# Optimization experiments

Measured on AMD Instinct MI355X. Metric: run time of the kernel, lower is better.

The kernel has to match this reference:

```python
import jax, jax.numpy as jnp
import numpy as np

GRID_SIZE = 5
SPLINE_ORDER = 3
N_COEF = GRID_SIZE + SPLINE_ORDER  # 8
NUM_NODES = 100000
NUM_EDGES = 1200000
NUM_GRAPHS = 512
D = 64
N_TARGETS = 10


def _grid():
    # uniform grid on [-1, 1] extended by spline_order knots on each side (efficient-kan default)
    h = 2.0 / GRID_SIZE
    return jnp.arange(-SPLINE_ORDER, GRID_SIZE + SPLINE_ORDER + 1, dtype=jnp.float32) * h - 1.0


def b_splines(x):
    # x: (N, in) -> (N, in, N_COEF) via Cox-de Boor recursion
    g = _grid()
    xe = x[..., None]
    bases = ((xe >= g[:-1]) & (xe < g[1:])).astype(x.dtype)
    for k in range(1, SPLINE_ORDER + 1):
        left = (xe - g[: -(k + 1)]) / (g[k:-1] - g[: -(k + 1)])
        right = (g[k + 1:] - xe) / (g[k + 1:] - g[1:-k])
        bases = left * bases[..., :-1] + right * bases[..., 1:]
    return bases


def kan_linear(x, base_w, spline_w, scaler):
    # efficient-kan KANLinear: silu base branch + standalone-scaled spline branch
    base = jax.nn.silu(x) @ base_w.T
    sb = b_splines(x)  # (N, in, N_COEF)
    spline = jnp.einsum('nig,oig->no', sb, spline_w * scaler[..., None])
    return base + spline


def setup_inputs() -> dict:
    key = jax.random.key(0)
    ks = jax.random.split(key, 12)
    inp = {
        'x': jax.random.normal(ks[0], (NUM_NODES, D), dtype=jnp.float32),
        'edge_index': jax.random.randint(ks[1], (2, NUM_EDGES), 0, NUM_NODES, dtype=jnp.int64),
        'batch': jnp.sort(jax.random.randint(ks[2], (NUM_NODES,), 0, NUM_GRAPHS, dtype=jnp.int64)),
        # GINConv layer 0 KAN (D -> D)
        'base_w0': jax.random.normal(ks[3], (D, D), dtype=jnp.float32) * 0.1,
        'spline_w0': jax.random.normal(ks[4], (D, D, N_COEF), dtype=jnp.float32) * 0.1,
        'scaler0': jax.random.normal(ks[5], (D, D), dtype=jnp.float32) * 0.1 + 1.0,
        # GINConv layer 1 KAN (D -> D)
        'base_w1': jax.random.normal(ks[6], (D, D), dtype=jnp.float32) * 0.1,
        'spline_w1': jax.random.normal(ks[7], (D, D, N_COEF), dtype=jnp.float32) * 0.1,
        'scaler1': jax.random.normal(ks[8], (D, D), dtype=jnp.float32) * 0.1 + 1.0,
        # head KAN (D -> N_TARGETS)
        'base_wh': jax.random.normal(ks[9], (N_TARGETS, D), dtype=jnp.float32) * 0.1,
        'spline_wh': jax.random.normal(ks[10], (N_TARGETS, D, N_COEF), dtype=jnp.float32) * 0.1,
        'scaler_h': jax.random.normal(ks[11], (N_TARGETS, D), dtype=jnp.float32) * 0.1 + 1.0,
    }
    return inp


def reference(x, edge_index, batch, base_w0, spline_w0, scaler0,
              base_w1, spline_w1, scaler1, base_wh, spline_wh, scaler_h):
    src, dst = edge_index[0], edge_index[1]
    n = x.shape[0]
    # GINConv layer 0: nn((1+eps)*x + sum_{j in N(i)} x_j), eps=0; dropout is eval-mode identity
    agg = jax.ops.segment_sum(x[src], dst, num_segments=n)
    h = kan_linear(x + agg, base_w0, spline_w0, scaler0)
    # GINConv layer 1
    agg = jax.ops.segment_sum(h[src], dst, num_segments=n)
    h = kan_linear(h + agg, base_w1, spline_w1, scaler1)
    # global_add_pool over graphs, then KAN head
    pooled = jax.ops.segment_sum(h, batch, num_segments=NUM_GRAPHS)
    return kan_linear(pooled, base_wh, spline_wh, scaler_h)
```

## Files before the change

kernel.cpp:

```cpp
#include <hip/hip_runtime.h>
#include <hip/hip_fp16.h>
#include <math.h>

#define NODES   100000
#define EDGES   1200000
#define GRAPHS  512
#define DIM     64
#define NT      10
#define KTOT    576

#define NB      512
#define NBUSED  391
#define EPB     4096
#define CAP     4608

#define KSTAGE     64
#define WTL_STRIDE 72
#define V_STRIDE   72

#define S3B     ((EDGES + EPB - 1) / EPB)
#define PREPB   ((2 * DIM * KTOT) / 512)
#define CONVB   ((NODES * 16 + 32 + 511) / 512)

typedef _Float16 f16x8  __attribute__((ext_vector_type(8)));
typedef __fp16   fp16x2 __attribute__((ext_vector_type(2)));
typedef __attribute__((ext_vector_type(4))) float frag_cd;

__device__ __forceinline__ float silu(float x) {
    return x * __builtin_amdgcn_rcpf(1.f + __expf(-x));
}

__device__ __forceinline__ unsigned packh2(float a, float b) {
    fp16x2 h = __builtin_amdgcn_cvt_pkrtz(a, b);
    return __builtin_bit_cast(unsigned, h);
}

union H8 { uint4 u; __half2 h[4]; };

__device__ __forceinline__ f16x8 bases_frag(float xv) {
    float tt  = fmaf(xv, 2.5f, 5.5f);
    float fm  = floorf(tt);
    int   m   = (int)fm;
    float u   = tt - fm;
    float u2  = u * u;
    float u3  = u2 * u;
    float v0  = fmaf(fmaf(fmaf(u, -(1.f / 6.f), 0.5f), u, -0.5f), u, 1.f / 6.f);
    float v1  = fmaf(u3, 0.5f, fmaf(u2, -1.f, 2.f / 3.f));
    float v2  = fmaf(u + u2 - u3, 0.5f, 1.f / 6.f);
    float v3  = u3 * (1.f / 6.f);

    unsigned d0 = packh2(v0, v1);
    unsigned d1 = packh2(v2, v3);
    int p = m - 3;
    int B = p >> 1;
    bool odd = (p & 1) != 0;
    unsigned e1 = __builtin_amdgcn_alignbit(d1, d0, 16);
    unsigned W0 = odd ? (d0 << 16) : d0;
    unsigned W1 = odd ? e1 : d1;
    unsigned W2 = odd ? (d1 >> 16) : 0u;
    union { f16x8 f; unsigned u[4]; } r;
    r.u[0] = (B == 0) ? W0 : ((B == -1) ? W1 : ((B == -2) ? W2 : 0u));
    r.u[1] = (B == 1) ? W0 : ((B ==  0) ? W1 : ((B == -1) ? W2 : 0u));
    r.u[2] = (B == 2) ? W0 : ((B ==  1) ? W1 : ((B ==  0) ? W2 : 0u));
    r.u[3] = (B == 3) ? W0 : ((B ==  2) ? W1 : ((B ==  1) ? W2 : 0u));
    return r.f;
}

__global__ __launch_bounds__(512) void mega(const int* __restrict__ ei,
                                            int* __restrict__ bcur,
                                            unsigned* __restrict__ tmp,
                                            const float* __restrict__ bw0,
                                            const float* __restrict__ sw0,
                                            const float* __restrict__ sc0,
                                            const float* __restrict__ bw1,
                                            const float* __restrict__ sw1,
                                            const float* __restrict__ sc1,
                                            unsigned short* __restrict__ wt0,
                                            unsigned short* __restrict__ wt1,
                                            const float* __restrict__ x,
                                            const int* __restrict__ bat,
                                            unsigned short* __restrict__ xb,
                                            unsigned short* __restrict__ hpad,
                                            int* __restrict__ goff) {
    __shared__ int hist[NB], lstart[NB], gbase[NB], cur[NB];
    __shared__ unsigned ebuf[EPB];
    __shared__ unsigned short bk[EPB];
    const int bx = blockIdx.x;
    const int t  = threadIdx.x;

    if (bx < S3B) {
        hist[t] = 0; cur[t] = 0;
        __syncthreads();
        const int e0 = bx * EPB;
        int src[8], dst[8];
#pragma unroll
        for (int k = 0; k < 8; ++k) {
            int e = e0 + t + k * 512;
            bool valid = e < EDGES;
            src[k] = valid ? ei[e] : 0;
            dst[k] = valid ? ei[EDGES + e] : -1;
            if (valid) atomicAdd(&hist[dst[k] >> 8], 1);
        }
        __syncthreads();
        int v = hist[t];
        lstart[t] = v;
        __syncthreads();
        int run = v;
        for (int d = 1; d < NB; d <<= 1) {
            int a = (t >= d) ? lstart[t - d] : 0;
            __syncthreads();
            run += a; lstart[t] = run;
            __syncthreads();
        }
        lstart[t] = run - v;
        if (v) gbase[t] = atomicAdd(&bcur[t], v);
        __syncthreads();
#pragma unroll
        for (int k = 0; k < 8; ++k) {
            if (dst[k] >= 0) {
                int b = dst[k] >> 8;
                int pos = lstart[b] + atomicAdd(&cur[b], 1);
                ebuf[pos] = (unsigned)src[k] | ((unsigned)(dst[k] & 255) << 24);
                bk[pos] = (unsigned short)b;
            }
        }
        __syncthreads();
        int total = EDGES - e0; if (total > EPB) total = EPB;
        for (int i = t; i < total; i += 512) {
            int b = bk[i];
            tmp[(size_t)b * CAP + gbase[b] + (i - lstart[b])] = ebuf[i];
        }
        return;
    }

    if (bx < S3B + PREPB) {
        int idx = (bx - S3B) * 512 + t;
        int layer = idx >= DIM * KTOT;
        int li = layer ? idx - DIM * KTOT : idx;
        const float* bw = layer ? bw1 : bw0;
        const float* sw = layer ? sw1 : sw0;
        const float* sc = layer ? sc1 : sc0;
        unsigned short* wt = layer ? wt1 : wt0;
        int o = li / KTOT, k = li % KTOT;
        float v;
        if (k < DIM) {
            v = bw[o * DIM + k];
        } else {
            int i = (k - DIM) >> 3, g = (k - DIM) & 7;
            v = sw[(o * DIM + i) * 8 + g] * sc[o * DIM + i];
        }
        wt[li] = __half_as_ushort(__float2half(v));
        return;
    }

    int i = (bx - S3B - PREPB) * 512 + t;
    if (i < NODES * 16) {
        float4 v = ((const float4*)x)[i];
        unsigned lo = packh2(v.x, v.y);
        unsigned hi = packh2(v.z, v.w);
        ((uint2*)xb)[i] = make_uint2(lo, hi);
        if ((i & 15) == 0) {
            int n = i >> 4;
            int b  = bat[n];
            int bp = (n == 0) ? -1 : bat[n - 1];
            for (int g = bp + 1; g <= b; ++g) goff[g] = n;
        }
        if (i == 0) {
            int blast = bat[NODES - 1];
            for (int g = blast + 1; g <= GRAPHS; ++g) goff[g] = NODES;
        }
    } else {
        int j = i - NODES * 16;
        if (j < 16)      ((uint2*)xb)[NODES * 16 + j] = make_uint2(0, 0);
        else if (j < 32) ((uint2*)hpad)[j - 16]       = make_uint2(0, 0);
    }
}

__global__ __launch_bounds__(1024) void s4_fill(const unsigned* __restrict__ tmp,
                                                const int* __restrict__ bcur,
                                                int2* __restrict__ rowp,
                                                int* __restrict__ col) {
    __shared__ int deg[256], scanI[256], cur[256];
    __shared__ int tot;
    __shared__ int4 colbuf4[CAP / 4];
    int* colbuf = (int*)colbuf4;
    const int b = blockIdx.x, t = threadIdx.x;
    const int cnt = bcur[b];
    const int base = b * CAP;
    if (t < 256) deg[t] = 0;
    __syncthreads();
    for (int i = t; i < cnt; i += 1024)
        atomicAdd(&deg[tmp[base + i] >> 24], 1);
    __syncthreads();
    if (t < 256) scanI[t] = (deg[t] + 3) & ~3;
    __syncthreads();
    for (int d = 1; d < 256; d <<= 1) {
        int a = 0;
        if (t < 256 && t >= d) a = scanI[t - d];
        __syncthreads();
        if (t < 256) scanI[t] += a;
        __syncthreads();
    }
    if (t < 256) {
        int pad = (deg[t] + 3) & ~3;
        int start = scanI[t] - pad;
        int ng = b * 256 + t;
        if (ng < NODES) rowp[ng] = make_int2(base + start, base + start + pad);
        cur[t] = start;
        if (t == 255) tot = scanI[255];
    }
    __syncthreads();
    for (int i = t; i < cnt; i += 1024) {
        unsigned p = tmp[base + i];
        int pos = atomicAdd(&cur[p >> 24], 1);
        colbuf[pos] = (int)(p & 0xFFFFFFu);
    }
    __syncthreads();
    if (t < 256) {
        int pad = (deg[t] + 3) & ~3;
        int end = scanI[t] - pad + pad;
        for (int k = cur[t]; k < end; ++k) colbuf[k] = NODES;
    }
    __syncthreads();
    int nq = tot >> 2;
    int4* out4 = (int4*)(col + base);
    for (int i = t; i < nq; i += 1024) out4[i] = colbuf4[i];
    if (t < 4) col[base + tot + t] = NODES;
}

__global__ __launch_bounds__(256, 8) void fused_layer(const unsigned short* __restrict__ xin,
                                                      const int2* __restrict__ rowp,
                                                      const int* __restrict__ col,
                                                      const unsigned short* __restrict__ wt,
                                                      unsigned short* __restrict__ out) {
    __shared__ unsigned short wt_lds[64 * WTL_STRIDE];
    __shared__ unsigned short v_lds[64 * V_STRIDE];

    const int t     = threadIdx.x;
    const int nbase = blockIdx.x * 64;

    uint4 p0, p1;
    {
        int c0 = t, c1 = t + 256;
        p0 = *(const uint4*)(wt + (c0 >> 3) * KTOT + (c0 & 7) * 8);
        p1 = *(const uint4*)(wt + (c1 >> 3) * KTOT + (c1 & 7) * 8);
    }

    const uint4* x4 = (const uint4*)xin;
#pragma unroll
    for (int rd = 0; rd < 2; ++rd) {
        int idx  = t + rd * 256;
        int node = idx >> 3, c8 = idx & 7;
        int n = nbase + node;
        uint4 res = make_uint4(0, 0, 0, 0);
        if (n < NODES) {
            int2 be = rowp[n];
            H8 a0, a1, a2, a3;
            a0.u = x4[n * 8 + c8];
            a1.u = make_uint4(0, 0, 0, 0);
            a2.u = make_uint4(0, 0, 0, 0);
            a3.u = make_uint4(0, 0, 0, 0);
            for (int p = be.x; p < be.y; p += 4) {
                int4 c4 = *(const int4*)(col + p);
                H8 r0, r1, r2, r3;
                r0.u = x4[c4.x * 8 + c8];
                r1.u = x4[c4.y * 8 + c8];
                r2.u = x4[c4.z * 8 + c8];
                r3.u = x4[c4.w * 8 + c8];
#pragma unroll
                for (int j = 0; j < 4; ++j) {
                    a0.h[j] = __hadd2(a0.h[j], r0.h[j]);
                    a1.h[j] = __hadd2(a1.h[j], r1.h[j]);
                    a2.h[j] = __hadd2(a2.h[j], r2.h[j]);
                    a3.h[j] = __hadd2(a3.h[j], r3.h[j]);
                }
            }
#pragma unroll
            for (int j = 0; j < 4; ++j)
                a0.h[j] = __hadd2(__hadd2(a0.h[j], a1.h[j]), __hadd2(a2.h[j], a3.h[j]));
            res = a0.u;
        }
        *(uint4*)(v_lds + node * V_STRIDE + c8 * 8) = res;
    }
    {
        int c0 = t, c1 = t + 256;
        *(uint4*)(wt_lds + (c0 >> 3) * WTL_STRIDE + (c0 & 7) * 8) = p0;
        *(uint4*)(wt_lds + (c1 >> 3) * WTL_STRIDE + (c1 & 7) * 8) = p1;
    }
    __syncthreads();

    const int w = t >> 6;
    const int l = t & 63;
    const int q = l >> 4;
    const int c = l & 15;
    const unsigned short* vrow = v_lds + ((w << 4) + c) * V_STRIDE;

    frag_cd ac0 = {0.f, 0.f, 0.f, 0.f};
    frag_cd ac1 = {0.f, 0.f, 0.f, 0.f};
    frag_cd ac2 = {0.f, 0.f, 0.f, 0.f};
    frag_cd ac3 = {0.f, 0.f, 0.f, 0.f};

#define MSTEP(OFF, A) {                                                          \
        f16x8 b0 = *(const f16x8*)(wt_lds + (c     ) * WTL_STRIDE + (OFF));      \
        f16x8 b1 = *(const f16x8*)(wt_lds + (c + 16) * WTL_STRIDE + (OFF));      \
        f16x8 b2 = *(const f16x8*)(wt_lds + (c + 32) * WTL_STRIDE + (OFF));      \
        f16x8 b3 = *(const f16x8*)(wt_lds + (c + 48) * WTL_STRIDE + (OFF));      \
        ac0 = __builtin_amdgcn_mfma_f32_16x16x32_f16(A, b0, ac0, 0, 0, 0);       \
        ac1 = __builtin_amdgcn_mfma_f32_16x16x32_f16(A, b1, ac1, 0, 0, 0);       \
        ac2 = __builtin_amdgcn_mfma_f32_16x16x32_f16(A, b2, ac2, 0, 0, 0);       \
        ac3 = __builtin_amdgcn_mfma_f32_16x16x32_f16(A, b3, ac3, 0, 0, 0); }

    {
        int c0 = t, c1 = t + 256;
        p0 = *(const uint4*)(wt + (c0 >> 3) * KTOT + KSTAGE + (c0 & 7) * 8);
        p1 = *(const uint4*)(wt + (c1 >> 3) * KTOT + KSTAGE + (c1 & 7) * 8);
    }

#pragma unroll
    for (int s = 0; s < 2; ++s) {
        f16x8 hv = *(const f16x8*)(vrow + 32 * s + 8 * q);
        float f[8];
#pragma unroll
        for (int j = 0; j < 8; ++j) f[j] = silu((float)hv[j]);
        union { f16x8 v; unsigned u[4]; } a;
#pragma unroll
        for (int j = 0; j < 4; ++j) a.u[j] = packh2(f[2 * j], f[2 * j + 1]);
        MSTEP(32 * s + 8 * q, a.v);
    }

#pragma unroll
    for (int st = 1; st < 9; ++st) {
        __syncthreads();
        {
            int c0 = t, c1 = t + 256;
            *(uint4*)(wt_lds + (c0 >> 3) * WTL_STRIDE + (c0 & 7) * 8) = p0;
            *(uint4*)(wt_lds + (c1 >> 3) * WTL_STRIDE + (c1 & 7) * 8) = p1;
        }
        __syncthreads();
        if (st < 8) {
            int c0 = t, c1 = t + 256;
            p0 = *(const uint4*)(wt + (c0 >> 3) * KTOT + (st + 1) * KSTAGE + (c0 & 7) * 8);
            p1 = *(const uint4*)(wt + (c1 >> 3) * KTOT + (st + 1) * KSTAGE + (c1 & 7) * 8);
        }
#pragma unroll
        for (int k2 = 0; k2 < 2; ++k2) {
            f16x8 a = bases_frag((float)(*(const _Float16*)(vrow + 8 * (st - 1) + 4 * k2 + q)));
            MSTEP(32 * k2 + 8 * q, a);
        }
    }
#undef MSTEP

    const int n0 = nbase + (w << 4) + (q << 2);
#pragma unroll
    for (int r = 0; r < 4; ++r) {
        int n = n0 + r;
        if (n < NODES) {
            unsigned short* o = out + (size_t)n * DIM + c;
            o[0]  = __half_as_ushort(__float2half(ac0[r]));
            o[16] = __half_as_ushort(__float2half(ac1[r]));
            o[32] = __half_as_ushort(__float2half(ac2[r]));
            o[48] = __half_as_ushort(__float2half(ac3[r]));
        }
    }
}

__global__ __launch_bounds__(256) void pool_head(const unsigned short* __restrict__ h,
                                                 const int* __restrict__ goff,
                                                 const float* __restrict__ bwh,
                                                 const float* __restrict__ swh,
                                                 const float* __restrict__ sch,
                                                 float* __restrict__ out) {
    __shared__ float red[32][64];
    const int g = blockIdx.x, t = threadIdx.x;
    const int start = goff[g], end = goff[g + 1];
    const int grp = t >> 3, c8 = t & 7;
    const uint4* h4 = (const uint4*)h;

    float f[8];
#pragma unroll
    for (int j = 0; j < 8; ++j) f[j] = 0.f;
    for (int n = start + grp; n < end; n += 32) {
        H8 v; v.u = h4[n * 8 + c8];
#pragma unroll
        for (int j = 0; j < 4; ++j) {
            float2 fj = __half22float2(v.h[j]);
            f[2 * j]     += fj.x;
            f[2 * j + 1] += fj.y;
        }
    }
#pragma unroll
    for (int j = 0; j < 8; ++j) red[grp][c8 * 8 + j] = f[j];
    __syncthreads();

    if (t < 64) {
        const int i = t;
        float xv = 0.f;
#pragma unroll
        for (int k = 0; k < 32; ++k) xv += red[k][i];

        float s  = silu(xv);
        float tt  = fmaf(xv, 2.5f, 5.5f);
        float fm  = floorf(tt);
        int   m   = (int)fm;
        float u   = tt - fm;
        float u2  = u * u;
        float u3  = u2 * u;
        float v0  = fmaf(fmaf(fmaf(u, -(1.f / 6.f), 0.5f), u, -0.5f), u, 1.f / 6.f);
        float v1  = fmaf(u3, 0.5f, fmaf(u2, -1.f, 2.f / 3.f));
        float v2  = fmaf(u + u2 - u3, 0.5f, 1.f / 6.f);
        float v3  = u3 * (1.f / 6.f);
        bool inr  = (m >= 0) && (m <= 10);
        float b[8];
#pragma unroll
        for (int j = 0; j < 8; ++j) {
            float bv = 0.f;
            bv = (j == m - 3) ? v0 : bv;
            bv = (j == m - 2) ? v1 : bv;
            bv = (j == m - 1) ? v2 : bv;
            bv = (j == m)     ? v3 : bv;
            b[j] = inr ? bv : 0.f;
        }

        float part[NT];
#pragma unroll
        for (int o = 0; o < NT; ++o) {
            const float* sp = swh + (o * DIM + i) * 8;
            float sb = 0.f;
#pragma unroll
            for (int qq = 0; qq < 8; ++qq) sb = fmaf(b[qq], sp[qq], sb);
            part[o] = fmaf(s, bwh[o * DIM + i], sb * sch[o * DIM + i]);
        }
#pragma unroll
        for (int o = 0; o < NT; ++o) {
            float v = part[o];
#pragma unroll
            for (int off = 32; off > 0; off >>= 1) v += __shfl_down(v, off, 64);
            if (i == 0) out[g * NT + o] = v;
        }
    }
}

extern "C" void kernel_launch(void* const* d_in, const int* in_sizes, int n_in,
                              void* d_out, int out_size, void* d_ws, size_t ws_size,
                              hipStream_t stream) {
    const float* x   = (const float*)d_in[0];
    const int*   ei  = (const int*)d_in[1];
    const int*   bat = (const int*)d_in[2];
    const float* bw0 = (const float*)d_in[3];
    const float* sw0 = (const float*)d_in[4];
    const float* sc0 = (const float*)d_in[5];
    const float* bw1 = (const float*)d_in[6];
    const float* sw1 = (const float*)d_in[7];
    const float* sc1 = (const float*)d_in[8];
    const float* bwh = (const float*)d_in[9];
    const float* swh = (const float*)d_in[10];
    const float* sch = (const float*)d_in[11];
    float* out = (float*)d_out;

    const size_t ROW = (size_t)(NODES + 1) * DIM;

    unsigned short* wt0 = (unsigned short*)d_ws;
    unsigned short* wt1 = wt0 + DIM * KTOT;
    unsigned short* xbf = wt1 + DIM * KTOT;
    unsigned short* hbf = xbf + ROW;
    unsigned short* h2  = hbf + ROW;
    int* goff     = (int*)(h2 + (size_t)NODES * DIM);
    int2* rowp    = (int2*)(goff + 514);
    int* col      = (int*)(rowp + NODES);
    int* bcur     = col + (size_t)NB * CAP;
    unsigned* tmp = (unsigned*)(bcur + NB);

    (void)hipMemsetAsync(bcur, 0, NB * sizeof(int), stream);

    mega<<<S3B + PREPB + CONVB, 512, 0, stream>>>(
        ei, bcur, tmp,
        bw0, sw0, sc0, bw1, sw1, sc1, wt0, wt1,
        x, bat, xbf, hbf + (size_t)NODES * DIM, goff);

    s4_fill<<<NBUSED, 1024, 0, stream>>>(tmp, bcur, rowp, col);

    const int layer_blocks = (NODES + 63) / 64;
    fused_layer<<<layer_blocks, 256, 0, stream>>>(xbf, rowp, col, wt0, hbf);
    fused_layer<<<layer_blocks, 256, 0, stream>>>(hbf, rowp, col, wt1, h2);

    pool_head<<<GRAPHS, 256, 0, stream>>>(h2, goff, bwh, swh, sch, out);
}
```

Before: 198.4 us.

## Replace bucketed LDS edge sort with global-atomic degree count, scan, and scatter CSR

Replaces the two-pass bucketed CSR build with a simpler three-step scheme. Per-node degrees are counted with global atomics inside the mega kernel. A wave-shuffle scan then computes padded row starts per 256-node block, and a separate scatter kernel places source indices using per-node atomic cursors. This removes the LDS histogram/scan/staging and the intermediate tmp buffer, at the cost of an extra kernel launch, many contended global atomics, random global writes, and nondeterministic neighbor order within a row.

```diff
diff --git a/kernel.cpp b/kernel.cpp
--- a/kernel.cpp
+++ b/kernel.cpp
@@ -67,8 +67,7 @@
 }
 
 __global__ __launch_bounds__(512) void mega(const int* __restrict__ ei,
-                                            int* __restrict__ bcur,
-                                            unsigned* __restrict__ tmp,
+                                            int* __restrict__ deg,
                                             const float* __restrict__ bw0,
                                             const float* __restrict__ sw0,
                                             const float* __restrict__ sc0,
@@ -82,53 +81,15 @@
                                             unsigned short* __restrict__ xb,
                                             unsigned short* __restrict__ hpad,
                                             int* __restrict__ goff) {
-    __shared__ int hist[NB], lstart[NB], gbase[NB], cur[NB];
-    __shared__ unsigned ebuf[EPB];
-    __shared__ unsigned short bk[EPB];
     const int bx = blockIdx.x;
     const int t  = threadIdx.x;
 
     if (bx < S3B) {
-        hist[t] = 0; cur[t] = 0;
-        __syncthreads();
-        const int e0 = bx * EPB;
-        int src[8], dst[8];
+        const int e0 = bx * EPB + t;
 #pragma unroll
         for (int k = 0; k < 8; ++k) {
-            int e = e0 + t + k * 512;
-            bool valid = e < EDGES;
-            src[k] = valid ? ei[e] : 0;
-            dst[k] = valid ? ei[EDGES + e] : -1;
-            if (valid) atomicAdd(&hist[dst[k] >> 8], 1);
-        }
-        __syncthreads();
-        int v = hist[t];
-        lstart[t] = v;
-        __syncthreads();
-        int run = v;
-        for (int d = 1; d < NB; d <<= 1) {
-            int a = (t >= d) ? lstart[t - d] : 0;
-            __syncthreads();
-            run += a; lstart[t] = run;
-            __syncthreads();
-        }
-        lstart[t] = run - v;
-        if (v) gbase[t] = atomicAdd(&bcur[t], v);
-        __syncthreads();
-#pragma unroll
-        for (int k = 0; k < 8; ++k) {
-            if (dst[k] >= 0) {
-                int b = dst[k] >> 8;
-                int pos = lstart[b] + atomicAdd(&cur[b], 1);
-                ebuf[pos] = (unsigned)src[k] | ((unsigned)(dst[k] & 255) << 24);
-                bk[pos] = (unsigned short)b;
-            }
-        }
-        __syncthreads();
-        int total = EDGES - e0; if (total > EPB) total = EPB;
-        for (int i = t; i < total; i += 512) {
-            int b = bk[i];
-            tmp[(size_t)b * CAP + gbase[b] + (i - lstart[b])] = ebuf[i];
+            int e = e0 + k * 512;
+            if (e < EDGES) atomicAdd(&deg[ei[EDGES + e]], 1);
         }
         return;
     }
@@ -176,56 +137,51 @@
     }
 }
 
-__global__ __launch_bounds__(1024) void s4_fill(const unsigned* __restrict__ tmp,
-                                                const int* __restrict__ bcur,
-                                                int2* __restrict__ rowp,
-                                                int* __restrict__ col) {
-    __shared__ int deg[256], scanI[256], cur[256];
-    __shared__ int tot;
-    __shared__ int4 colbuf4[CAP / 4];
-    int* colbuf = (int*)colbuf4;
+__global__ __launch_bounds__(256) void s4p(const int* __restrict__ deg,
+                                           int2* __restrict__ rowp,
+                                           int* __restrict__ cur,
+                                           int* __restrict__ col) {
+    __shared__ int wsum[4];
     const int b = blockIdx.x, t = threadIdx.x;
-    const int cnt = bcur[b];
-    const int base = b * CAP;
-    if (t < 256) deg[t] = 0;
+    const int ng = b * 256 + t;
+    const int d   = (ng < NODES) ? deg[ng] : 0;
+    const int pad = (d + 3) & ~3;
+
+    int v = pad;
+#pragma unroll
+    for (int off = 1; off < 64; off <<= 1) {
+        int u = __shfl_up(v, off, 64);
+        if ((t & 63) >= off) v += u;
+    }
+    const int wid = t >> 6;
+    if ((t & 63) == 63) wsum[wid] = v;
     __syncthreads();
-    for (int i = t; i < cnt; i += 1024)
-        atomicAdd(&deg[tmp[base + i] >> 24], 1);
-    __syncthreads();
-    if (t < 256) scanI[t] = (deg[t] + 3) & ~3;
-    __syncthreads();
-    for (int d = 1; d < 256; d <<= 1) {
-        int a = 0;
-        if (t < 256 && t >= d) a = scanI[t - d];
-        __syncthreads();
-        if (t < 256) scanI[t] += a;
-        __syncthreads();
-    }
-    if (t < 256) {
-        int pad = (deg[t] + 3) & ~3;
-        int start = scanI[t] - pad;
-        int ng = b * 256 + t;
-        if (ng < NODES) rowp[ng] = make_int2(base + start, base + start + pad);
-        cur[t] = start;
-        if (t == 255) tot = scanI[255];
-    }
-    __syncthreads();
-    for (int i = t; i < cnt; i += 1024) {
-        unsigned p = tmp[base + i];
-        int pos = atomicAdd(&cur[p >> 24], 1);
-        colbuf[pos] = (int)(p & 0xFFFFFFu);
-    }
-    __syncthreads();
-    if (t < 256) {
-        int pad = (deg[t] + 3) & ~3;
-        int end = scanI[t] - pad + pad;
-        for (int k = cur[t]; k < end; ++k) colbuf[k] = NODES;
-    }
-    __syncthreads();
-    int nq = tot >> 2;
-    int4* out4 = (int4*)(col + base);
-    for (int i = t; i < nq; i += 1024) out4[i] = colbuf4[i];
-    if (t < 4) col[base + tot + t] = NODES;
+    int wpre = 0;
+#pragma unroll
+    for (int k = 0; k < 3; ++k) if (k < wid) wpre += wsum[k];
+
+    if (ng < NODES) {
+        int start = b * CAP + wpre + v - pad;
+        rowp[ng] = make_int2(start, start + pad);
+        cur[ng]  = start;
+        for (int k = d; k < pad; ++k) col[start + k] = NODES;
+    }
+}
+
+__global__ __launch_bounds__(512) void scat(const int* __restrict__ ei,
+                                            int* __restrict__ cur,
+                                            int* __restrict__ col) {
+    const int e0 = blockIdx.x * EPB + threadIdx.x;
+#pragma unroll
+    for (int k = 0; k < 8; ++k) {
+        int e = e0 + k * 512;
+        if (e < EDGES) {
+            int s  = ei[e];
+            int dn = ei[EDGES + e];
+            int pos = atomicAdd(&cur[dn], 1);
+            col[pos] = s;
+        }
+    }
 }
 
 __global__ __launch_bounds__(256, 8) void fused_layer(const unsigned short* __restrict__ xin,
@@ -467,17 +423,19 @@
     int* goff     = (int*)(h2 + (size_t)NODES * DIM);
     int2* rowp    = (int2*)(goff + 514);
     int* col      = (int*)(rowp + NODES);
-    int* bcur     = col + (size_t)NB * CAP;
-    unsigned* tmp = (unsigned*)(bcur + NB);
-
-    (void)hipMemsetAsync(bcur, 0, NB * sizeof(int), stream);
+    int* deg      = col + (size_t)NB * CAP;
+    int* cur      = deg + NODES;
+
+    (void)hipMemsetAsync(deg, 0, NODES * sizeof(int), stream);
 
     mega<<<S3B + PREPB + CONVB, 512, 0, stream>>>(
-        ei, bcur, tmp,
+        ei, deg,
         bw0, sw0, sc0, bw1, sw1, sc1, wt0, wt1,
         x, bat, xbf, hbf + (size_t)NODES * DIM, goff);
 
-    s4_fill<<<NBUSED, 1024, 0, stream>>>(tmp, bcur, rowp, col);
+    s4p<<<NBUSED, 256, 0, stream>>>(deg, rowp, cur, col);
+
+    scat<<<S3B, 512, 0, stream>>>(ei, cur, col);
 
     const int layer_blocks = (NODES + 63) / 64;
     fused_layer<<<layer_blocks, 256, 0, stream>>>(xbf, rowp, col, wt0, hbf);
```

Measured after the change: 326.9 us. +64.8%, slower.
